# Kernel tuning notes

Measured on AMD Instinct MI355X. Metric: run time of the kernel, lower is better.

## Reference

```python
import jax, jax.numpy as jnp
import numpy as np

N_NODES = 100000
N_EDGES = 1600000
IN_DIM = 128
HEADS = 8
HEAD_DIM = 16  # output_dim 128 / heads 8
NEG_SLOPE = 0.2  # PyG GATConv default LeakyReLU slope


def setup_inputs() -> dict:
    key = jax.random.key(0)
    k1, k2, k3, k4, k5 = jax.random.split(key, 5)
    x = jax.random.normal(k1, (N_NODES, IN_DIM), dtype=jnp.float32)
    edge_index = jax.random.randint(k2, (2, N_EDGES), 0, N_NODES, dtype=jnp.int64)
    scale = 1.0 / np.sqrt(IN_DIM)
    W = jax.random.normal(k3, (IN_DIM, HEADS * HEAD_DIM), dtype=jnp.float32) * scale
    a_src = jax.random.normal(k4, (HEADS, HEAD_DIM), dtype=jnp.float32) * scale
    a_dst = jax.random.normal(k5, (HEADS, HEAD_DIM), dtype=jnp.float32) * scale
    bias = jnp.zeros((HEADS * HEAD_DIM,), dtype=jnp.float32)
    return {"x": x, "edge_index": edge_index, "W": W, "a_src": a_src, "a_dst": a_dst, "bias": bias}


def reference(x, edge_index, W, a_src, a_dst, bias):
    N = x.shape[0]
    H, D = a_src.shape
    # add self-loops (PyG GATConv default add_self_loops=True)
    loop = jnp.arange(N, dtype=edge_index.dtype)
    src = jnp.concatenate([edge_index[0], loop])  # message sources j
    dst = jnp.concatenate([edge_index[1], loop])  # message targets i

    h = (x @ W).reshape(N, H, D)  # per-head projected features
    alpha_src = jnp.sum(h * a_src, axis=-1)  # [N, H]
    alpha_dst = jnp.sum(h * a_dst, axis=-1)  # [N, H]

    # edge-wise attention logits, softmax over incoming edges of each dst node
    e = jax.nn.leaky_relu(alpha_src[src] + alpha_dst[dst], NEG_SLOPE)  # [E', H]
    e_max = jax.ops.segment_max(e, dst, num_segments=N)
    e_exp = jnp.exp(e - e_max[dst])
    denom = jax.ops.segment_sum(e_exp, dst, num_segments=N)
    alpha = e_exp / (denom[dst] + 1e-16)  # [E', H]

    # weighted scatter-sum of source features
    out = jax.ops.segment_sum(alpha[:, :, None] * h[src], dst, num_segments=N)  # [N, H, D]
    out = out.reshape(N, H * D) + bias
    # wrapper: ReLU (concat=True), dropout is identity in eval mode
    return jax.nn.relu(out)
```

## Files before the change

### kernel.cpp

```cpp
#include <hip/hip_runtime.h>
#include <hip/hip_bf16.h>

#define NEG_SLOPE 0.2f
#define NBUCK 782
#define ABLK 8192
#define CAP 3072

typedef __attribute__((ext_vector_type(8))) short bf16x8v;
typedef __attribute__((ext_vector_type(4))) float f32x4;
typedef __attribute__((ext_vector_type(2))) float f32x2;

__device__ __forceinline__ unsigned f2bf_bits(float f) {
    unsigned u = __float_as_uint(f);
    return (u + 0x7fffu + ((u >> 16) & 1u)) >> 16;
}
__device__ __forceinline__ float bflo(unsigned u) { return __uint_as_float(u << 16); }
__device__ __forceinline__ float bfhi(unsigned u) { return __uint_as_float(u & 0xffff0000u); }

__device__ __forceinline__ void pkfma(f32x2& a, f32x2 x, f32x2 w) {
    asm("v_pk_fma_f32 %0, %1, %2, %0" : "+v"(a) : "v"(x), "v"(w));
}

__global__ __launch_bounds__(256) void prep_w(const float* __restrict__ W,
                                              const float* __restrict__ a_src,
                                              const float* __restrict__ a_dst,
                                              short* __restrict__ WtE) {
    int id = blockIdx.x * 256 + threadIdx.x;
    if (id >= 144 * 128) return;
    int n = id >> 7, k = id & 127;
    float v;
    if (n < 128) {
        v = W[k * 128 + n];
    } else if (n < 136) {
        int hh = n - 128; float s = 0.f;
#pragma unroll
        for (int d = 0; d < 16; ++d) s += W[k * 128 + hh * 16 + d] * a_src[hh * 16 + d];
        v = s;
    } else {
        int hh = n - 136; float s = 0.f;
#pragma unroll
        for (int d = 0; d < 16; ++d) s += W[k * 128 + hh * 16 + d] * a_dst[hh * 16 + d];
        v = s;
    }
    WtE[id] = (short)f2bf_bits(v);
}

__global__ __launch_bounds__(256) void gemm_mfma(const float* __restrict__ x,
                                                 const short* __restrict__ WtE,
                                                 short* __restrict__ hout,
                                                 float* __restrict__ as,
                                                 float* __restrict__ ad, int N) {
    __shared__ short xs[64 * 136];
    __shared__ short wt[144 * 136];
    const int tid = threadIdx.x;
    const int r0 = blockIdx.x * 64;

#pragma unroll
    for (int p = 0; p < 9; ++p) {
        int idx = p * 256 + tid;
        int n = idx >> 4, kk = (idx & 15) * 8;
        *(uint4*)&wt[n * 136 + kk] = *(const uint4*)(WtE + n * 128 + kk);
    }
#pragma unroll
    for (int p = 0; p < 8; ++p) {
        int lin = p * 1024 + tid * 4;
        int row = lin >> 7, k = lin & 127;
        int gr = r0 + row;
        int grc = gr < N ? gr : N - 1;
        float4 v = *(const float4*)(x + (size_t)grc * 128 + k);
        unsigned p0 = f2bf_bits(v.x) | (f2bf_bits(v.y) << 16);
        unsigned p1 = f2bf_bits(v.z) | (f2bf_bits(v.w) << 16);
        *(uint2*)&xs[row * 136 + k] = make_uint2(p0, p1);
    }
    __syncthreads();

    const int wv = tid >> 6;
    const int lane = tid & 63;
    const int lc = lane & 15, quad = lane >> 4;
    f32x4 acc[9];
#pragma unroll
    for (int c = 0; c < 9; ++c) acc[c] = (f32x4){0.f, 0.f, 0.f, 0.f};
    const short* aB = &xs[(wv * 16 + lc) * 136 + quad * 8];
    const short* bB = &wt[lc * 136 + quad * 8];
#pragma unroll
    for (int kc = 0; kc < 4; ++kc) {
        bf16x8v af = *(const bf16x8v*)(aB + kc * 32);
#pragma unroll
        for (int c = 0; c < 9; ++c) {
            bf16x8v bf = *(const bf16x8v*)(bB + c * (16 * 136) + kc * 32);
            acc[c] = __builtin_amdgcn_mfma_f32_16x16x32_bf16(af, bf, acc[c], 0, 0, 0);
        }
    }

    const int rowb = r0 + wv * 16 + quad * 4;
#pragma unroll
    for (int c = 0; c < 8; ++c) {
#pragma unroll
        for (int r = 0; r < 4; ++r) {
            int row = rowb + r;
            if (row < N) hout[(size_t)row * 128 + c * 16 + lc] = (short)f2bf_bits(acc[c][r]);
        }
    }
#pragma unroll
    for (int r = 0; r < 4; ++r) {
        int row = rowb + r;
        if (row < N) {
            if (lc < 8) as[row * 8 + lc] = acc[8][r];
            else        ad[row * 8 + (lc - 8)] = acc[8][r];
        }
    }
}

__global__ __launch_bounds__(1024) void bucket_edges(const int* __restrict__ ei, int E,
                                                     unsigned* __restrict__ slab,
                                                     int* __restrict__ cntG,
                                                     int* __restrict__ startG) {
    __shared__ int hist[1024];
    __shared__ int cur[NBUCK];
    __shared__ int wpart[16];
    const int t = threadIdx.x;
    const int blk = blockIdx.x;
    const int base = blk * ABLK;
    int count = E - base; if (count > ABLK) count = ABLK;

    int sr[8], dr[8];
    hist[t] = 0;
#pragma unroll
    for (int k = 0; k < 8; ++k) {
        int i = k * 1024 + t;
        if (i < count) { sr[k] = ei[base + i]; dr[k] = ei[E + base + i]; }
    }
    __syncthreads();
#pragma unroll
    for (int k = 0; k < 8; ++k) {
        int i = k * 1024 + t;
        if (i < count) atomicAdd(&hist[dr[k] >> 7], 1);
    }
    __syncthreads();
    int v = hist[t];
    int lane = t & 63, wid = t >> 6;
    int sc = v;
#pragma unroll
    for (int off = 1; off < 64; off <<= 1) { int u = __shfl_up(sc, off); if (lane >= off) sc += u; }
    if (lane == 63) wpart[wid] = sc;
    __syncthreads();
    if (wid == 0 && lane < 16) {
        int wv = wpart[lane], wsum = wv;
#pragma unroll
        for (int off = 1; off < 16; off <<= 1) { int u = __shfl_up(wsum, off); if (lane >= off) wsum += u; }
        wpart[lane] = wsum - wv;
    }
    __syncthreads();
    int excl = sc - v + wpart[wid];
    if (t < NBUCK) {
        cntG[blk * NBUCK + t]   = v;
        startG[blk * NBUCK + t] = excl;
        cur[t] = excl;
    }
    __syncthreads();
#pragma unroll
    for (int k = 0; k < 8; ++k) {
        int i = k * 1024 + t;
        if (i < count) {
            int d = dr[k];
            int pos = atomicAdd(&cur[d >> 7], 1);
            slab[(size_t)blk * ABLK + pos] = (unsigned)sr[k] | ((unsigned)(d & 127) << 17);
        }
    }
}

__global__ __launch_bounds__(512) void build_csr(const unsigned* __restrict__ slab,
                                                 const int* __restrict__ cntG,
                                                 const int* __restrict__ startG,
                                                 int nblk, int N,
                                                 int* __restrict__ rowS,
                                                 int* __restrict__ rowE,
                                                 int* __restrict__ sortedSrc) {
    __shared__ int eL[CAP];
    __shared__ int incl[512];
    __shared__ int cS[512];
    __shared__ int stS[512];
    __shared__ int lp[128];
    __shared__ int wpart[8];
    __shared__ int halfSum;
    const int bb = blockIdx.x;
    const int t = threadIdx.x;
    const int nodeBase = bb << 7;
    const int bBase = bb * CAP;

    int c = 0, st = 0;
    if (t < nblk) { c = cntG[t * NBUCK + bb]; st = startG[t * NBUCK + bb]; }
    cS[t] = c; stS[t] = st;
    if (t < 128) lp[t] = 0;
    int lane = t & 63, wid = t >> 6;
    int sc = c;
#pragma unroll
    for (int off = 1; off < 64; off <<= 1) { int u = __shfl_up(sc, off); if (lane >= off) sc += u; }
    if (lane == 63) wpart[wid] = sc;
    __syncthreads();
    if (wid == 0 && lane < 8) {
        int wv = wpart[lane], wsum = wv;
#pragma unroll
        for (int off = 1; off < 8; off <<= 1) { int u = __shfl_up(wsum, off); if (lane >= off) wsum += u; }
        wpart[lane] = wsum - wv;
    }
    __syncthreads();
    incl[t] = sc + wpart[wid];
    __syncthreads();
    int total = incl[511];
    if (total > CAP) total = CAP;
    for (int s = wid; s < nblk; s += 8) {
        int cc = cS[s];
        int off0 = incl[s] - cc;
        const unsigned* p = slab + (size_t)s * ABLK + stS[s];
        for (int i = lane; i < cc; i += 64) eL[off0 + i] = (int)p[i];
    }
    __syncthreads();
    for (int e = t; e < total; e += 512) atomicAdd(&lp[((unsigned)eL[e]) >> 17], 1);
    __syncthreads();
    int cnt = 0, s2 = 0;
    if (t < 128) {
        cnt = lp[t];
        s2 = cnt;
#pragma unroll
        for (int off = 1; off < 64; off <<= 1) { int u = __shfl_up(s2, off); if (lane >= off) s2 += u; }
        if (t == 63) halfSum = s2;
    }
    __syncthreads();
    if (t < 128) {
        int inc2 = s2 + (t >= 64 ? halfSum : 0);
        int ex = inc2 - cnt;
        int gn = nodeBase + t;
        if (gn < N) { rowS[gn] = bBase + ex; rowE[gn] = bBase + ex + cnt; }
        lp[t] = ex;
    }
    __syncthreads();
    for (int e = t; e < total; e += 512) {
        unsigned pk = (unsigned)eL[e];
        int pos = atomicAdd(&lp[pk >> 17], 1);
        sortedSrc[bBase + pos] = (int)(pk & 0x1FFFFu);
    }
}

__global__ __launch_bounds__(256, 6) void aggregate(const int* __restrict__ rowS,
                                                    const int* __restrict__ rowE,
                                                    const int* __restrict__ sortedSrc,
                                                    const short* __restrict__ h,
                                                    const float* __restrict__ as,
                                                    const float* __restrict__ ad,
                                                    const float* __restrict__ bias,
                                                    float* __restrict__ out, int N) {
    const int wv = __builtin_amdgcn_readfirstlane((int)(threadIdx.x >> 6));
    const int node = blockIdx.x * 4 + wv;
    if (node >= N) return;
    const int lane = threadIdx.x & 63;
    const int g = lane >> 3, p = lane & 7;
    const int start = rowS[node], end = rowE[node];
    const float adv = ad[node * 8 + p];
    const short* hb = h + p * 16;

    f32x2 acc[8];
#pragma unroll
    for (int k = 0; k < 8; ++k) acc[k] = (f32x2){0.f, 0.f};
    float dsum = 0.f;

    float as0 = 0.f, as1 = 0.f, as2 = 0.f;
    uint4 hA0 = {0,0,0,0}, hA1 = {0,0,0,0};
    uint4 hB0 = {0,0,0,0}, hB1 = {0,0,0,0};
    uint4 hC0 = {0,0,0,0}, hC1 = {0,0,0,0};

#define SLOT_LOAD(EV, ASV, H0, H1)                                  \
    if ((EV) < end) {                                               \
        int j = sortedSrc[EV];                                      \
        ASV = as[j * 8 + p];                                        \
        const uint4* hp = (const uint4*)(hb + (size_t)j * 128);     \
        H0 = hp[0]; H1 = hp[1];                                     \
    }

#define EDGE_COMPUTE(ASV, H0, H1)                                   \
    {                                                               \
        float tt = ASV + adv;                                       \
        tt = tt > 0.f ? tt : NEG_SLOPE * tt;                        \
        float w = __expf(tt);                                       \
        f32x2 wp = {w, w};                                          \
        f32x2 tv;                                                   \
        tv.x = bflo(H0.x); tv.y = bfhi(H0.x); pkfma(acc[0], tv, wp); \
        tv.x = bflo(H0.y); tv.y = bfhi(H0.y); pkfma(acc[1], tv, wp); \
        tv.x = bflo(H0.z); tv.y = bfhi(H0.z); pkfma(acc[2], tv, wp); \
        tv.x = bflo(H0.w); tv.y = bfhi(H0.w); pkfma(acc[3], tv, wp); \
        tv.x = bflo(H1.x); tv.y = bfhi(H1.x); pkfma(acc[4], tv, wp); \
        tv.x = bflo(H1.y); tv.y = bfhi(H1.y); pkfma(acc[5], tv, wp); \
        tv.x = bflo(H1.z); tv.y = bfhi(H1.z); pkfma(acc[6], tv, wp); \
        tv.x = bflo(H1.w); tv.y = bfhi(H1.w); pkfma(acc[7], tv, wp); \
        dsum += w;                                                  \
    }

    int e = start + g;
    SLOT_LOAD(e, as0, hA0, hA1)
    SLOT_LOAD(e + 8, as1, hB0, hB1)
    SLOT_LOAD(e + 16, as2, hC0, hC1)

    while (e < end) {
        EDGE_COMPUTE(as0, hA0, hA1)
        SLOT_LOAD(e + 24, as0, hA0, hA1)
        if (e + 8 < end) EDGE_COMPUTE(as1, hB0, hB1)
        SLOT_LOAD(e + 32, as1, hB0, hB1)
        if (e + 16 < end) EDGE_COMPUTE(as2, hC0, hC1)
        SLOT_LOAD(e + 40, as2, hC0, hC1)
        e += 24;
    }

#pragma unroll
    for (int m = 8; m <= 32; m <<= 1) {
#pragma unroll
        for (int k = 0; k < 8; ++k) {
            acc[k].x += __shfl_xor(acc[k].x, m);
            acc[k].y += __shfl_xor(acc[k].y, m);
        }
        dsum += __shfl_xor(dsum, m);
    }
    {
        float slas = as[node * 8 + p];
        const uint4* hp = (const uint4*)(hb + (size_t)node * 128);
        uint4 s0 = hp[0], s1 = hp[1];
        EDGE_COMPUTE(slas, s0, s1)
    }
    if (g == 0) {
        float inv = 1.0f / (dsum + 1e-16f);
        float* op = out + (size_t)node * 128 + p * 16;
        const float* bp = bias + p * 16;
#pragma unroll
        for (int q = 0; q < 4; ++q) {
            float4 bv = *(const float4*)(bp + q * 4);
            float o0 = acc[2 * q].x     * inv + bv.x;
            float o1 = acc[2 * q].y     * inv + bv.y;
            float o2 = acc[2 * q + 1].x * inv + bv.z;
            float o3 = acc[2 * q + 1].y * inv + bv.w;
            o0 = o0 > 0.f ? o0 : 0.f; o1 = o1 > 0.f ? o1 : 0.f;
            o2 = o2 > 0.f ? o2 : 0.f; o3 = o3 > 0.f ? o3 : 0.f;
            *(float4*)(op + q * 4) = make_float4(o0, o1, o2, o3);
        }
    }
#undef SLOT_LOAD
#undef EDGE_COMPUTE
}

extern "C" void kernel_launch(void* const* d_in, const int* in_sizes, int n_in,
                              void* d_out, int out_size, void* d_ws, size_t ws_size,
                              hipStream_t stream) {
    const float* x     = (const float*)d_in[0];
    const int*   ei    = (const int*)d_in[1];
    const float* W     = (const float*)d_in[2];
    const float* a_src = (const float*)d_in[3];
    const float* a_dst = (const float*)d_in[4];
    const float* bias  = (const float*)d_in[5];
    float* out = (float*)d_out;

    const int N = in_sizes[0] / 128;
    const int E = in_sizes[1] / 2;
    const int nblk = (E + ABLK - 1) / ABLK;

    char* ws = (char*)d_ws;
    size_t off = 0;
    auto alloc = [&](size_t bytes) { void* p = ws + off; off = (off + bytes + 255) & ~(size_t)255; return p; };
    short*    h         = (short*)alloc((size_t)N * 128 * 2);
    float*    as        = (float*)alloc((size_t)N * 8 * 4);
    float*    ad        = (float*)alloc((size_t)N * 8 * 4);
    unsigned* slab      = (unsigned*)alloc((size_t)nblk * ABLK * 4);
    int*      cntG      = (int*)alloc((size_t)nblk * NBUCK * 4);
    int*      startG    = (int*)alloc((size_t)nblk * NBUCK * 4);
    int*      sortedSrc = (int*)alloc((size_t)NBUCK * CAP * 4);
    int*      rowS      = (int*)alloc((size_t)N * 4);
    int*      rowE      = (int*)alloc((size_t)N * 4);
    short*    WtE       = (short*)alloc((size_t)144 * 128 * 2);

    prep_w<<<72, 256, 0, stream>>>(W, a_src, a_dst, WtE);
    gemm_mfma<<<(N + 63) / 64, 256, 0, stream>>>(x, WtE, h, as, ad, N);
    bucket_edges<<<nblk, 1024, 0, stream>>>(ei, E, slab, cntG, startG);
    build_csr<<<NBUCK, 512, 0, stream>>>(slab, cntG, startG, nblk, N, rowS, rowE, sortedSrc);
    aggregate<<<(N + 3) / 4, 256, 0, stream>>>(rowS, rowE, sortedSrc, h, as, ad, bias, out, N);
}
```

Baseline: 233.5 us.

## Fuse weight prep into bucketing kernel, pack count/start, regroup slab copy

Merges the prep_w weight-transform work into extra blocks of the bucket_edges launch, which removes one kernel launch and reorders the stream so bucketing runs before the GEMM. Count and start arrays are packed into one int2 array so build_csr reads a single coalesced value. The slab-to-LDS copy in build_csr now uses 8-lane groups per source block instead of 64-lane waves, since per-bucket counts are small (about 10). The aggregate kernel also gets a short-row fast path that skips the loop and its prefetch loads for nodes with 24 or fewer edges.

Result: faster. 227.7 us (-2.5%).

```diff
diff --git a/kernel.cpp b/kernel.cpp
--- a/kernel.cpp
+++ b/kernel.cpp
@@ -19,30 +19,6 @@
 
 __device__ __forceinline__ void pkfma(f32x2& a, f32x2 x, f32x2 w) {
     asm("v_pk_fma_f32 %0, %1, %2, %0" : "+v"(a) : "v"(x), "v"(w));
-}
-
-__global__ __launch_bounds__(256) void prep_w(const float* __restrict__ W,
-                                              const float* __restrict__ a_src,
-                                              const float* __restrict__ a_dst,
-                                              short* __restrict__ WtE) {
-    int id = blockIdx.x * 256 + threadIdx.x;
-    if (id >= 144 * 128) return;
-    int n = id >> 7, k = id & 127;
-    float v;
-    if (n < 128) {
-        v = W[k * 128 + n];
-    } else if (n < 136) {
-        int hh = n - 128; float s = 0.f;
-#pragma unroll
-        for (int d = 0; d < 16; ++d) s += W[k * 128 + hh * 16 + d] * a_src[hh * 16 + d];
-        v = s;
-    } else {
-        int hh = n - 136; float s = 0.f;
-#pragma unroll
-        for (int d = 0; d < 16; ++d) s += W[k * 128 + hh * 16 + d] * a_dst[hh * 16 + d];
-        v = s;
-    }
-    WtE[id] = (short)f2bf_bits(v);
 }
 
 __global__ __launch_bounds__(256) void gemm_mfma(const float* __restrict__ x,
@@ -112,14 +88,42 @@
 }
 
 __global__ __launch_bounds__(1024) void bucket_edges(const int* __restrict__ ei, int E,
+                                                     int nblk,
                                                      unsigned* __restrict__ slab,
-                                                     int* __restrict__ cntG,
-                                                     int* __restrict__ startG) {
+                                                     int2* __restrict__ csG,
+                                                     const float* __restrict__ W,
+                                                     const float* __restrict__ a_src,
+                                                     const float* __restrict__ a_dst,
+                                                     short* __restrict__ WtE) {
+    const int t = threadIdx.x;
+    const int blk = blockIdx.x;
+
+    if (blk >= nblk) {
+        int id = (blk - nblk) * 1024 + t;
+        if (id < 144 * 128) {
+            int n = id >> 7, k = id & 127;
+            float v;
+            if (n < 128) {
+                v = W[k * 128 + n];
+            } else if (n < 136) {
+                int hh = n - 128; float s = 0.f;
+#pragma unroll
+                for (int d = 0; d < 16; ++d) s += W[k * 128 + hh * 16 + d] * a_src[hh * 16 + d];
+                v = s;
+            } else {
+                int hh = n - 136; float s = 0.f;
+#pragma unroll
+                for (int d = 0; d < 16; ++d) s += W[k * 128 + hh * 16 + d] * a_dst[hh * 16 + d];
+                v = s;
+            }
+            WtE[id] = (short)f2bf_bits(v);
+        }
+        return;
+    }
+
     __shared__ int hist[1024];
     __shared__ int cur[NBUCK];
     __shared__ int wpart[16];
-    const int t = threadIdx.x;
-    const int blk = blockIdx.x;
     const int base = blk * ABLK;
     int count = E - base; if (count > ABLK) count = ABLK;
 
@@ -153,8 +157,7 @@
     __syncthreads();
     int excl = sc - v + wpart[wid];
     if (t < NBUCK) {
-        cntG[blk * NBUCK + t]   = v;
-        startG[blk * NBUCK + t] = excl;
+        csG[(size_t)blk * NBUCK + t] = make_int2(v, excl);
         cur[t] = excl;
     }
     __syncthreads();
@@ -170,8 +173,7 @@
 }
 
 __global__ __launch_bounds__(512) void build_csr(const unsigned* __restrict__ slab,
-                                                 const int* __restrict__ cntG,
-                                                 const int* __restrict__ startG,
+                                                 const int2* __restrict__ csG,
                                                  int nblk, int N,
                                                  int* __restrict__ rowS,
                                                  int* __restrict__ rowE,
@@ -189,7 +191,7 @@
     const int bBase = bb * CAP;
 
     int c = 0, st = 0;
-    if (t < nblk) { c = cntG[t * NBUCK + bb]; st = startG[t * NBUCK + bb]; }
+    if (t < nblk) { int2 cs = csG[(size_t)t * NBUCK + bb]; c = cs.x; st = cs.y; }
     cS[t] = c; stS[t] = st;
     if (t < 128) lp[t] = 0;
     int lane = t & 63, wid = t >> 6;
@@ -209,11 +211,14 @@
     __syncthreads();
     int total = incl[511];
     if (total > CAP) total = CAP;
-    for (int s = wid; s < nblk; s += 8) {
-        int cc = cS[s];
-        int off0 = incl[s] - cc;
-        const unsigned* p = slab + (size_t)s * ABLK + stS[s];
-        for (int i = lane; i < cc; i += 64) eL[off0 + i] = (int)p[i];
+    {
+        const int grp = t >> 3, li = t & 7;
+        for (int s = grp; s < nblk; s += 64) {
+            int cc = cS[s];
+            int off0 = incl[s] - cc;
+            const unsigned* p = slab + (size_t)s * ABLK + stS[s];
+            for (int i = li; i < cc; i += 8) eL[off0 + i] = (int)p[i];
+        }
     }
     __syncthreads();
     for (int e = t; e < total; e += 512) atomicAdd(&lp[((unsigned)eL[e]) >> 17], 1);
@@ -300,14 +305,20 @@
     SLOT_LOAD(e + 8, as1, hB0, hB1)
     SLOT_LOAD(e + 16, as2, hC0, hC1)
 
-    while (e < end) {
-        EDGE_COMPUTE(as0, hA0, hA1)
-        SLOT_LOAD(e + 24, as0, hA0, hA1)
-        if (e + 8 < end) EDGE_COMPUTE(as1, hB0, hB1)
-        SLOT_LOAD(e + 32, as1, hB0, hB1)
+    if (end - start <= 24) {
+        if (e < end)      EDGE_COMPUTE(as0, hA0, hA1)
+        if (e + 8 < end)  EDGE_COMPUTE(as1, hB0, hB1)
         if (e + 16 < end) EDGE_COMPUTE(as2, hC0, hC1)
-        SLOT_LOAD(e + 40, as2, hC0, hC1)
-        e += 24;
+    } else {
+        while (e < end) {
+            EDGE_COMPUTE(as0, hA0, hA1)
+            SLOT_LOAD(e + 24, as0, hA0, hA1)
+            if (e + 8 < end) EDGE_COMPUTE(as1, hB0, hB1)
+            SLOT_LOAD(e + 32, as1, hB0, hB1)
+            if (e + 16 < end) EDGE_COMPUTE(as2, hC0, hC1)
+            SLOT_LOAD(e + 40, as2, hC0, hC1)
+            e += 24;
+        }
     }
 
 #pragma unroll
@@ -367,16 +378,14 @@
     float*    as        = (float*)alloc((size_t)N * 8 * 4);
     float*    ad        = (float*)alloc((size_t)N * 8 * 4);
     unsigned* slab      = (unsigned*)alloc((size_t)nblk * ABLK * 4);
-    int*      cntG      = (int*)alloc((size_t)nblk * NBUCK * 4);
-    int*      startG    = (int*)alloc((size_t)nblk * NBUCK * 4);
+    int2*     csG       = (int2*)alloc((size_t)nblk * NBUCK * 8);
     int*      sortedSrc = (int*)alloc((size_t)NBUCK * CAP * 4);
     int*      rowS      = (int*)alloc((size_t)N * 4);
     int*      rowE      = (int*)alloc((size_t)N * 4);
     short*    WtE       = (short*)alloc((size_t)144 * 128 * 2);
 
-    prep_w<<<72, 256, 0, stream>>>(W, a_src, a_dst, WtE);
+    bucket_edges<<<nblk + 18, 1024, 0, stream>>>(ei, E, nblk, slab, csG, W, a_src, a_dst, WtE);
     gemm_mfma<<<(N + 63) / 64, 256, 0, stream>>>(x, WtE, h, as, ad, N);
-    bucket_edges<<<nblk, 1024, 0, stream>>>(ei, E, slab, cntG, startG);
-    build_csr<<<NBUCK, 512, 0, stream>>>(slab, cntG, startG, nblk, N, rowS, rowE, sortedSrc);
+    build_csr<<<NBUCK, 512, 0, stream>>>(slab, csG, nblk, N, rowS, rowE, sortedSrc);
     aggregate<<<(N + 3) / 4, 256, 0, stream>>>(rowS, rowE, sortedSrc, h, as, ad, bias, out, N);
 }
```
